# Kernel tuning notes

Hardware: AMD Instinct MI355X
Metric: run time of the kernel (lower is better)

## Reference

```python
import jax, jax.numpy as jnp
import numpy as np

B, S = 4, 2048
DM, H, DK, DV, DI = 512, 4, 128, 128, 1024
NT, NV = 64, 5000
PAD = 0


def layernorm(x, g, b, eps=1e-5):
    m = jnp.mean(x, axis=-1, keepdims=True)
    v = jnp.var(x, axis=-1, keepdims=True)
    return (x - m) * jax.lax.rsqrt(v + eps) * g + b


def setup_inputs() -> dict:
    key = jax.random.key(0)
    ks = jax.random.split(key, 20)
    event_type = jax.random.randint(ks[0], (B, S), 0, NT + 1)
    vertex = jax.random.randint(ks[1], (B, S), 0, NV + 1)
    vertex = jnp.where(event_type == PAD, 0, vertex)  # align padding
    event_time = jnp.sort(jax.random.uniform(ks[2], (B, S)) * 100.0, axis=1)
    non_pad_mask = (event_type != PAD).astype(jnp.float32)[..., None]  # [B,S,1]
    sc = 0.02
    event_emb = jax.random.normal(ks[3], (NT + 1, DM)) * sc
    event_emb = event_emb.at[PAD].set(0.0)
    vertex_emb = jax.random.normal(ks[4], (NV + 1, DM)) * sc
    vertex_emb = vertex_emb.at[PAD].set(0.0)
    A = jax.random.uniform(ks[5], (NV, NV))
    W = jax.random.uniform(ks[6], (NV, NV))
    Wq = jax.random.normal(ks[7], (DM, H * DK)) * sc
    Wk = jax.random.normal(ks[8], (DM, H * DK)) * sc
    Wv = jax.random.normal(ks[9], (DM, H * DV)) * sc
    Wo = jax.random.normal(ks[10], (H * DV, DM)) * sc
    bo = jnp.zeros((DM,))
    ln1_g, ln1_b = jnp.ones((DM,)), jnp.zeros((DM,))
    w1 = jax.random.normal(ks[11], (DM, DI)) * sc
    b1 = jnp.zeros((DI,))
    w2 = jax.random.normal(ks[12], (DI, DM)) * sc
    b2 = jnp.zeros((DM,))
    ln2_g, ln2_b = jnp.ones((DM,)), jnp.zeros((DM,))
    return dict(event_type=event_type, vertex=vertex, event_time=event_time,
                non_pad_mask=non_pad_mask, A=A, W=W, event_emb=event_emb,
                vertex_emb=vertex_emb, Wq=Wq, Wk=Wk, Wv=Wv, Wo=Wo, bo=bo,
                ln1_g=ln1_g, ln1_b=ln1_b, w1=w1, b1=b1, w2=w2, b2=b2,
                ln2_g=ln2_g, ln2_b=ln2_b)


def similarity(vertex, A, W):
    # vectorized form of the triple-loop pairwise gather: [B,1,S,S]
    idx = jnp.clip(vertex - 1, 0)                       # [B,S]
    vm = (vertex != 0)
    pair = vm[:, :, None] & vm[:, None, :]              # [B,S,S]
    sim = A[idx[:, :, None], idx[:, None, :]] * W[idx[:, :, None], idx[:, None, :]] * 10.0
    return (sim * pair.astype(A.dtype))[:, None]        # [B,1,S,S]


def temporal_enc(event_time, non_pad_mask, d_model):
    i = jnp.arange(d_model)
    pv = jnp.power(jnp.float32(10000.0), 2.0 * (i // 2).astype(jnp.float32) / d_model)
    r = event_time[:, :, None] / pv                     # [B,S,D]
    return jnp.where(i % 2 == 0, jnp.sin(r), jnp.cos(r)) * non_pad_mask


def reference(event_type, vertex, event_time, non_pad_mask, A, W, event_emb,
              vertex_emb, Wq, Wk, Wv, Wo, bo, ln1_g, ln1_b, w1, b1, w2, b2,
              ln2_g, ln2_b):
    b_, s_ = event_type.shape
    # masks: key-padding OR subsequent (causal)
    pad = (event_type == PAD)
    subseq = jnp.triu(jnp.ones((s_, s_), dtype=bool), 1)
    slf_attn_mask = pad[:, None, :] | subseq[None]      # [B,S,S]

    sim = similarity(vertex, A, W)                      # [B,1,S,S]
    tem = temporal_enc(event_time, non_pad_mask, DM)    # [B,S,D]
    ver = vertex_emb[vertex]                            # [B,S,D]
    enc = event_emb[event_type]                         # [B,S,D]

    # single encoder layer (n_layers=1), post-norm THP-style
    enc = enc + ver + tem
    res = enc
    q = (enc @ Wq).reshape(b_, s_, H, DK)
    k = (enc @ Wk).reshape(b_, s_, H, DK)
    v = (enc @ Wv).reshape(b_, s_, H, DV)
    scores = jnp.einsum('bihd,bjhd->bhij', q, k) / jnp.sqrt(jnp.float32(DK)) + sim
    scores = jnp.where(slf_attn_mask[:, None], jnp.float32(-1e9), scores)
    attn = jax.nn.softmax(scores, axis=-1)
    o = jnp.einsum('bhij,bjhd->bihd', attn, v).reshape(b_, s_, H * DV)
    o = o @ Wo + bo
    enc = layernorm(o + res, ln1_g, ln1_b) * non_pad_mask
    res = enc
    f = jax.nn.relu(enc @ w1 + b1) @ w2 + b2
    enc = layernorm(f + res, ln2_g, ln2_b) * non_pad_mask
    return enc, sim
```

## Files before the change

kernel.cpp:

```cpp
#include <hip/hip_runtime.h>
#include <hip/hip_bf16.h>

#define B_ 4
#define S_ 2048
#define DM_ 512
#define H_ 4
#define DK_ 128
#define DI_ 1024
#define NV_ 5000

typedef __attribute__((ext_vector_type(8))) short bf16x8;
typedef __attribute__((ext_vector_type(8))) unsigned short u16x8;
typedef __attribute__((ext_vector_type(4))) unsigned short u16x4;
typedef __attribute__((ext_vector_type(4))) float f32x4;

__device__ inline unsigned short f2bf(float x) {
  unsigned int u = __float_as_uint(x);
  unsigned int r = (u + 0x7fffu + ((u >> 16) & 1u)) >> 16;
  return (unsigned short)r;
}
__device__ inline float bf2f(unsigned short u) {
  return __uint_as_float(((unsigned int)u) << 16);
}
__device__ inline void gload16(const void* g, void* l) {
  __builtin_amdgcn_global_load_lds(
      (const __attribute__((address_space(1))) void*)g,
      (__attribute__((address_space(3))) void*)l, 16, 0, 0);
}

__global__ __launch_bounds__(256) void ew_kernel(
    const int* __restrict__ et, const int* __restrict__ vx,
    const float* __restrict__ tmv, const float* __restrict__ npm,
    const float* __restrict__ eemb, const float* __restrict__ vemb,
    const float* __restrict__ Wq, const float* __restrict__ Wk,
    const float* __restrict__ Wv, const float* __restrict__ Wo,
    const float* __restrict__ w1, const float* __restrict__ w2,
    float* __restrict__ enc0, unsigned short* __restrict__ enc0b,
    unsigned short* __restrict__ WqT, unsigned short* __restrict__ WkT,
    unsigned short* __restrict__ WvT, unsigned short* __restrict__ WoT,
    unsigned short* __restrict__ w1T, unsigned short* __restrict__ w2T) {
  __shared__ unsigned short T[32][40];
  int bid = blockIdx.x;
  int tid = threadIdx.x;
  if (bid < 8192) {
    int row = bid;
    int t = et[row], v = vx[row];
    float time = tmv[row], mask = npm[row];
    #pragma unroll
    for (int k = 0; k < 2; ++k) {
      int dd = tid + k * 256;
      float pvinv = __expf((float)(dd & ~1) * -0.017988946039015984f);
      float r = time * pvinv;
      float tem = (((dd & 1) == 0) ? sinf(r) : cosf(r)) * mask;
      float val = eemb[(size_t)t * DM_ + dd] + vemb[(size_t)v * DM_ + dd] + tem;
      enc0[(size_t)row * DM_ + dd] = val;
      enc0b[(size_t)row * DM_ + dd] = f2bf(val);
    }
  } else {
    int wb = bid - 8192;
    const float* src; unsigned short* dst; int K, N, lid;
    if (wb < 256)       { src = Wq; dst = WqT; K = 512;  N = 512;  lid = wb; }
    else if (wb < 512)  { src = Wk; dst = WkT; K = 512;  N = 512;  lid = wb - 256; }
    else if (wb < 768)  { src = Wv; dst = WvT; K = 512;  N = 512;  lid = wb - 512; }
    else if (wb < 1024) { src = Wo; dst = WoT; K = 512;  N = 512;  lid = wb - 768; }
    else if (wb < 1536) { src = w1; dst = w1T; K = 512;  N = 1024; lid = wb - 1024; }
    else                { src = w2; dst = w2T; K = 1024; N = 512;  lid = wb - 1536; }
    int nt = N / 32;
    int n0 = (lid % nt) * 32, k0 = (lid / nt) * 32;
    int r = tid >> 3, c0 = (tid & 7) * 4;
    float4 v = *(const float4*)&src[(size_t)(k0 + r) * N + n0 + c0];
    T[r][c0 + 0] = f2bf(v.x);
    T[r][c0 + 1] = f2bf(v.y);
    T[r][c0 + 2] = f2bf(v.z);
    T[r][c0 + 3] = f2bf(v.w);
    __syncthreads();
    u16x4 o;
    o[0] = T[c0 + 0][r]; o[1] = T[c0 + 1][r];
    o[2] = T[c0 + 2][r]; o[3] = T[c0 + 3][r];
    *(u16x4*)&dst[(size_t)(n0 + r) * K + k0 + c0] = o;
  }
}

__global__ __launch_bounds__(256) void simqkv_kernel(
    const int* __restrict__ vx, const float* __restrict__ A,
    const float* __restrict__ W, float* __restrict__ sim,
    const unsigned short* __restrict__ enc0b, const unsigned short* __restrict__ BT,
    unsigned short* __restrict__ QKV) {
  __shared__ __attribute__((aligned(16))) char arena[40960];
  int bid = blockIdx.x;
  int tid = threadIdx.x;
  int g = bid / 19, rr = bid % 19;
  if (rr < 16) {
    int job = g * 16 + rr;
    float* Ar = (float*)arena;
    float* Wr = (float*)(arena + 20480);
    int i = job & 2047;
    int b = job >> 11;
    int vi = vx[b * S_ + i];
    float* out = sim + ((size_t)(b * S_ + i)) * S_;
    if (vi == 0) {
      for (int j = tid * 4; j < S_; j += 1024)
        *(float4*)&out[j] = (float4){0.f, 0.f, 0.f, 0.f};
      return;
    }
    int w = tid >> 6, l = tid & 63;
    const char* Abase = (const char*)(A + (size_t)(vi - 1) * NV_);
    const char* Wbase = (const char*)(W + (size_t)(vi - 1) * NV_);
    #pragma unroll
    for (int it = 0; it < 5; ++it) {
      int seg = it * 4 + w;
      int chunk = seg * 64 + l;
      if (chunk < 1250) {
        gload16(Abase + (size_t)chunk * 16, (char*)Ar + seg * 1024);
        gload16(Wbase + (size_t)chunk * 16, (char*)Wr + seg * 1024);
      }
    }
    asm volatile("s_waitcnt vmcnt(0)" ::: "memory");
    __syncthreads();
    for (int j = tid * 4; j < S_; j += 1024) {
      int4 vj = *(const int4*)&vx[b * S_ + j];
      float4 o;
      o.x = vj.x ? Ar[vj.x - 1] * Wr[vj.x - 1] * 10.0f : 0.f;
      o.y = vj.y ? Ar[vj.y - 1] * Wr[vj.y - 1] * 10.0f : 0.f;
      o.z = vj.z ? Ar[vj.z - 1] * Wr[vj.z - 1] * 10.0f : 0.f;
      o.w = vj.w ? Ar[vj.w - 1] * Wr[vj.w - 1] * 10.0f : 0.f;
      *(float4*)&out[j] = o;
    }
  } else {
    unsigned short* As = (unsigned short*)arena;
    unsigned short* Bs = (unsigned short*)(arena + 9216);
    int qb = g * 3 + (rr - 16);
    int bx = qb % 12, by = qb / 12;
    int w = tid >> 6, l = tid & 63;
    int l16 = l & 15, lh = l >> 4;
    int row0 = by * 64, col0 = bx * 128;
    int ra = tid >> 1, ha = (tid & 1) * 32;
    int ra2 = tid >> 2, ha2 = (tid & 3) * 16;
    f32x4 acc[4][2];
    #pragma unroll
    for (int m = 0; m < 4; ++m)
      #pragma unroll
      for (int n = 0; n < 2; ++n) acc[m][n] = (f32x4){0.f, 0.f, 0.f, 0.f};

    for (int k0 = 0; k0 < 512; k0 += 64) {
      __syncthreads();
      {
        const unsigned short* sa = &enc0b[(size_t)(row0 + ra2) * 512 + k0 + ha2];
        uint4 a0 = *(const uint4*)(sa);
        uint4 a1 = *(const uint4*)(sa + 8);
        *(uint4*)&As[ra2 * 72 + ha2 + 0] = a0;
        *(uint4*)&As[ra2 * 72 + ha2 + 8] = a1;
        const unsigned short* sb = &BT[(size_t)(col0 + ra) * 512 + k0 + ha];
        uint4 b0 = *(const uint4*)(sb);
        uint4 b1 = *(const uint4*)(sb + 8);
        uint4 b2 = *(const uint4*)(sb + 16);
        uint4 b3 = *(const uint4*)(sb + 24);
        *(uint4*)&Bs[ra * 72 + ha + 0] = b0;
        *(uint4*)&Bs[ra * 72 + ha + 8] = b1;
        *(uint4*)&Bs[ra * 72 + ha + 16] = b2;
        *(uint4*)&Bs[ra * 72 + ha + 24] = b3;
      }
      __syncthreads();
      #pragma unroll
      for (int kc = 0; kc < 2; ++kc) {
        bf16x8 af[4], bfr[2];
        #pragma unroll
        for (int m = 0; m < 4; ++m)
          af[m] = *(bf16x8*)&As[(m * 16 + l16) * 72 + kc * 32 + lh * 8];
        #pragma unroll
        for (int n = 0; n < 2; ++n)
          bfr[n] = *(bf16x8*)&Bs[(w * 32 + n * 16 + l16) * 72 + kc * 32 + lh * 8];
        #pragma unroll
        for (int m = 0; m < 4; ++m)
          #pragma unroll
          for (int n = 0; n < 2; ++n)
            acc[m][n] = __builtin_amdgcn_mfma_f32_16x16x32_bf16(af[m], bfr[n], acc[m][n], 0, 0, 0);
      }
    }
    #pragma unroll
    for (int m = 0; m < 4; ++m) {
      #pragma unroll
      for (int r = 0; r < 4; ++r) {
        int row = row0 + m * 16 + lh * 4 + r;
        #pragma unroll
        for (int n = 0; n < 2; ++n) {
          int colg = col0 + w * 32 + n * 16 + l16;
          float v = acc[m][n][r];
          int which = colg >> 9;
          int cl = colg & 511;
          int b = row >> 11, s = row & 2047;
          int h = cl >> 7, d = cl & 127;
          unsigned short* base = QKV + (size_t)which * 4194304;
          if (which < 2)
            base[((size_t)((b * 4 + h) * 2048 + s)) * 128 + d] = f2bf(v);
          else
            base[((size_t)((b * 4 + h) * 128 + d)) * 2048 + s] = f2bf(v);
        }
      }
    }
  }
}

template <int OMODE, bool RELU, int MT = 128>
__global__ __launch_bounds__(256) void gemm_bf16_kernel(
    const unsigned short* __restrict__ A, const unsigned short* __restrict__ BT,
    const float* __restrict__ bias, void* __restrict__ C,
    int M, int N, int K) {
  __shared__ __attribute__((aligned(16))) unsigned short As[MT][72];
  __shared__ __attribute__((aligned(16))) unsigned short Bs[128][72];
  int tid = threadIdx.x;
  int w = tid >> 6, l = tid & 63;
  int l16 = l & 15, lh = l >> 4;
  const int NFR = (MT == 128) ? 4 : 2;
  int wr = (MT == 128) ? (w >> 1) : 0;
  int wc = (MT == 128) ? (w & 1) : w;
  int row0 = blockIdx.y * MT, col0 = blockIdx.x * 128;
  int ra = tid >> 1, ha = (tid & 1) * 32;
  f32x4 acc[4][4];
  #pragma unroll
  for (int m = 0; m < 4; ++m)
    #pragma unroll
    for (int n = 0; n < NFR; ++n) acc[m][n] = (f32x4){0.f, 0.f, 0.f, 0.f};

  for (int k0 = 0; k0 < K; k0 += 64) {
    __syncthreads();
    if (MT == 128) {
      const unsigned short* sa = &A[(size_t)(row0 + ra) * K + k0 + ha];
      uint4 a0 = *(const uint4*)(sa);
      uint4 a1 = *(const uint4*)(sa + 8);
      uint4 a2 = *(const uint4*)(sa + 16);
      uint4 a3 = *(const uint4*)(sa + 24);
      *(uint4*)&As[ra][ha + 0] = a0;
      *(uint4*)&As[ra][ha + 8] = a1;
      *(uint4*)&As[ra][ha + 16] = a2;
      *(uint4*)&As[ra][ha + 24] = a3;
    } else {
      int ra2 = tid >> 2, ha2 = (tid & 3) * 16;
      const unsigned short* sa = &A[(size_t)(row0 + ra2) * K + k0 + ha2];
      uint4 a0 = *(const uint4*)(sa);
      uint4 a1 = *(const uint4*)(sa + 8);
      *(uint4*)&As[ra2][ha2 + 0] = a0;
      *(uint4*)&As[ra2][ha2 + 8] = a1;
    }
    {
      const unsigned short* sb = &BT[(size_t)(col0 + ra) * K + k0 + ha];
      uint4 b0 = *(const uint4*)(sb);
      uint4 b1 = *(const uint4*)(sb + 8);
      uint4 b2 = *(const uint4*)(sb + 16);
      uint4 b3 = *(const uint4*)(sb + 24);
      *(uint4*)&Bs[ra][ha + 0] = b0;
      *(uint4*)&Bs[ra][ha + 8] = b1;
      *(uint4*)&Bs[ra][ha + 16] = b2;
      *(uint4*)&Bs[ra][ha + 24] = b3;
    }
    __syncthreads();
    #pragma unroll
    for (int kc = 0; kc < 2; ++kc) {
      bf16x8 af[4], bfr[4];
      #pragma unroll
      for (int m = 0; m < 4; ++m)
        af[m] = *(bf16x8*)&As[wr * 64 + m * 16 + l16][kc * 32 + lh * 8];
      #pragma unroll
      for (int n = 0; n < NFR; ++n)
        bfr[n] = *(bf16x8*)&Bs[wc * (16 * NFR) + n * 16 + l16][kc * 32 + lh * 8];
      #pragma unroll
      for (int m = 0; m < 4; ++m)
        #pragma unroll
        for (int n = 0; n < NFR; ++n)
          acc[m][n] = __builtin_amdgcn_mfma_f32_16x16x32_bf16(af[m], bfr[n], acc[m][n], 0, 0, 0);
    }
  }
  #pragma unroll
  for (int m = 0; m < 4; ++m) {
    #pragma unroll
    for (int r = 0; r < 4; ++r) {
      int row = row0 + wr * 64 + m * 16 + lh * 4 + r;
      #pragma unroll
      for (int n = 0; n < NFR; ++n) {
        int colg = col0 + wc * (16 * NFR) + n * 16 + l16;
        float v = acc[m][n][r];
        if (bias) v += bias[colg];
        if (RELU) v = fmaxf(v, 0.f);
        if (OMODE == 0) {
          ((float*)C)[(size_t)row * N + colg] = v;
        } else {
          ((unsigned short*)C)[(size_t)row * N + colg] = f2bf(v);
        }
      }
    }
  }
}

__global__ __launch_bounds__(256) void attn_mfma_kernel(
    const unsigned short* __restrict__ Qb, const unsigned short* __restrict__ Kb,
    const unsigned short* __restrict__ Vt, const float* __restrict__ sim,
    const float* __restrict__ npm, unsigned short* __restrict__ Op0,
    unsigned short* __restrict__ Op1, float2* __restrict__ ml0,
    float2* __restrict__ ml1) {
  __shared__ __attribute__((aligned(16))) char KsL[2][16384];
  __shared__ __attribute__((aligned(16))) char VtsL[2][16384];
  __shared__ __attribute__((aligned(16))) unsigned short Pl[4][16][72];
  int bid = blockIdx.x;
  int xcd = bid & 7;
  int j0 = bid >> 3;
  int bh = xcd * 2 + (j0 & 1);
  int jj = j0 >> 1;
  int pair = jj & 15;
  int half = jj >> 4;
  int b = bh >> 2;
  int tid = threadIdx.x;
  int w = tid >> 6, l = tid & 63;
  int l16 = l & 15, lh = l >> 4;
  unsigned short* Op = half ? Op1 : Op0;
  float2* ml = half ? ml1 : ml0;

  const char* KbB = (const char*)Kb + (size_t)bh * 2048 * 256;
  const char* VtB = (const char*)Vt + (size_t)bh * 128 * 4096;
  int krow[4], kcol[4], vrow4[4], vcol[4];
  #pragma unroll
  for (int j = 0; j < 4; ++j) {
    int i = w * 4 + j;
    krow[j] = i * 4 + (l >> 4);
    kcol[j] = ((l & 15) * 16) ^ ((krow[j] & 7) << 4);
    vrow4[j] = i * 8 + (l >> 3);
    vcol[j] = ((l & 7) * 16) ^ ((vrow4[j] & 7) << 4);
  }
  int xr = (l16 & 7) << 4;

  #pragma unroll 1
  for (int pj = 0; pj < 2; ++pj) {
    int qt = pj ? 31 - pair : pair;
    int nst = qt + 1;
    int c0 = (nst + 1) >> 1;
    int t0 = half ? c0 : 0;
    int cnt = half ? nst - c0 : c0;
    int q0 = qt * 64 + w * 16;
    int qg = q0 + l16;

    bf16x8 qf[4];
    const unsigned short* Qrow = Qb + ((size_t)(bh * 2048 + qg)) * 128;
    #pragma unroll
    for (int kq = 0; kq < 4; ++kq)
      qf[kq] = *(const bf16x8*)&Qrow[kq * 32 + lh * 8];

    float m_l = -INFINITY, l_l = 0.f;
    f32x4 o_acc[8];
    #pragma unroll
    for (int c = 0; c < 8; ++c) o_acc[c] = (f32x4){0.f, 0.f, 0.f, 0.f};

    const float* simrow = sim + ((size_t)(b * 2048) + qg) * 2048;
    const float* mrow = npm + b * 2048;

    if (cnt > 0) {
      #pragma unroll
      for (int j = 0; j < 4; ++j) {
        int i = w * 4 + j;
        gload16(KbB + (size_t)(t0 * 64 + krow[j]) * 256 + kcol[j],
                &KsL[0][i * 1024]);
        gload16(VtB + (size_t)vrow4[j] * 4096 + (size_t)(t0 * 64) * 2 + vcol[j],
                &VtsL[0][i * 1024]);
      }
      asm volatile("s_waitcnt vmcnt(0)" ::: "memory");
      __syncthreads();

      #pragma unroll 1
      for (int ti = 0; ti < cnt; ++ti) {
        int cur = ti & 1;
        int kv0 = (t0 + ti) * 64;
        if (ti + 1 < cnt) {
          int kvn = kv0 + 64;
          #pragma unroll
          for (int j = 0; j < 4; ++j) {
            int i = w * 4 + j;
            gload16(KbB + (size_t)(kvn + krow[j]) * 256 + kcol[j],
                    &KsL[cur ^ 1][i * 1024]);
            gload16(VtB + (size_t)vrow4[j] * 4096 + (size_t)kvn * 2 + vcol[j],
                    &VtsL[cur ^ 1][i * 1024]);
          }
        }
        const char* Kbase = KsL[cur];
        f32x4 sc[4];
        #pragma unroll
        for (int tt = 0; tt < 4; ++tt) {
          sc[tt] = (f32x4){0.f, 0.f, 0.f, 0.f};
          const char* Krow = Kbase + (tt * 16 + l16) * 256;
          #pragma unroll
          for (int kq = 0; kq < 4; ++kq) {
            bf16x8 kf = *(const bf16x8*)(Krow + ((kq * 64 + lh * 16) ^ xr));
            sc[tt] = __builtin_amdgcn_mfma_f32_16x16x32_bf16(kf, qf[kq], sc[tt], 0, 0, 0);
          }
        }
        float4 sim4[4], mk4[4];
        #pragma unroll
        for (int tt = 0; tt < 4; ++tt) {
          sim4[tt] = *(const float4*)&simrow[kv0 + tt * 16 + lh * 4];
          mk4[tt] = *(const float4*)&mrow[kv0 + tt * 16 + lh * 4];
        }
        float sv[4][4];
        #pragma unroll
        for (int tt = 0; tt < 4; ++tt) {
          #pragma unroll
          for (int r = 0; r < 4; ++r) {
            int kvg = kv0 + tt * 16 + lh * 4 + r;
            float mkr = r == 0 ? mk4[tt].x : r == 1 ? mk4[tt].y
                      : r == 2 ? mk4[tt].z : mk4[tt].w;
            float smr = r == 0 ? sim4[tt].x : r == 1 ? sim4[tt].y
                      : r == 2 ? sim4[tt].z : sim4[tt].w;
            bool valid = (kvg <= qg) && (mkr != 0.f);
            sv[tt][r] = valid ? sc[tt][r] * 0.08838834764831845f + smr : -1e9f;
          }
        }
        float mx = sv[0][0];
        #pragma unroll
        for (int tt = 0; tt < 4; ++tt)
          #pragma unroll
          for (int r = 0; r < 4; ++r) mx = fmaxf(mx, sv[tt][r]);
        mx = fmaxf(mx, __shfl_xor(mx, 16));
        mx = fmaxf(mx, __shfl_xor(mx, 32));
        float mn = fmaxf(m_l, mx);
        float alpha = __expf(m_l - mn);
        m_l = mn;
        float ts = 0.f;
        #pragma unroll
        for (int tt = 0; tt < 4; ++tt)
          #pragma unroll
          for (int r = 0; r < 4; ++r) {
            float ppv = __expf(sv[tt][r] - mn);
            sv[tt][r] = ppv;
            ts += ppv;
          }
        ts += __shfl_xor(ts, 16);
        ts += __shfl_xor(ts, 32);
        l_l = l_l * alpha + ts;
        #pragma unroll
        for (int tt = 0; tt < 4; ++tt) {
          u16x4 pw;
          pw[0] = f2bf(sv[tt][0]); pw[1] = f2bf(sv[tt][1]);
          pw[2] = f2bf(sv[tt][2]); pw[3] = f2bf(sv[tt][3]);
          *(u16x4*)&Pl[w][l16][tt * 16 + lh * 4] = pw;
        }
        float al[4];
        #pragma unroll
        for (int r = 0; r < 4; ++r) al[r] = __shfl(alpha, lh * 4 + r);
        #pragma unroll
        for (int c = 0; c < 8; ++c)
          #pragma unroll
          for (int r = 0; r < 4; ++r) o_acc[c][r] *= al[r];
        const char* Vbase = VtsL[cur];
        #pragma unroll
        for (int kf2 = 0; kf2 < 2; ++kf2) {
          bf16x8 pa = *(bf16x8*)&Pl[w][l16][kf2 * 32 + lh * 8];
          #pragma unroll
          for (int c = 0; c < 8; ++c) {
            bf16x8 vf = *(const bf16x8*)(Vbase + (c * 16 + l16) * 128 +
                                         ((kf2 * 64 + lh * 16) ^ xr));
            o_acc[c] = __builtin_amdgcn_mfma_f32_16x16x32_bf16(pa, vf, o_acc[c], 0, 0, 0);
          }
        }
        asm volatile("s_waitcnt vmcnt(0)" ::: "memory");
        __syncthreads();
      }
    }
    #pragma unroll
    for (int r = 0; r < 4; ++r) {
      int qgr = q0 + lh * 4 + r;
      unsigned short* op = Op + ((size_t)(bh * 2048 + qgr)) * 128;
      #pragma unroll
      for (int c = 0; c < 8; ++c) op[c * 16 + l16] = f2bf(o_acc[c][r]);
    }
    if (lh == 0) {
      float2 v; v.x = m_l; v.y = l_l;
      ml[bh * 2048 + q0 + l16] = v;
    }
    __syncthreads();
  }
}

__global__ __launch_bounds__(256) void attn_combine_kernel(
    const unsigned short* __restrict__ Op0, const unsigned short* __restrict__ Op1,
    const float2* __restrict__ ml0, const float2* __restrict__ ml1,
    unsigned short* __restrict__ Of) {
  int idx = blockIdx.x * 256 + threadIdx.x;
  int row = idx >> 4;
  int d0 = (idx & 15) * 8;
  float2 a = ml0[row], c2 = ml1[row];
  float m = fmaxf(a.x, c2.x);
  float e1 = __expf(a.x - m), e2 = __expf(c2.x - m);
  float inv = 1.f / (e1 * a.y + e2 * c2.y);
  u16x8 o1 = *(const u16x8*)&Op0[(size_t)row * 128 + d0];
  u16x8 o2 = *(const u16x8*)&Op1[(size_t)row * 128 + d0];
  int bh = row >> 11, q = row & 2047;
  int b = bh >> 2, h = bh & 3;
  unsigned short* dst = Of + ((size_t)(b * 2048 + q)) * 512 + h * 128 + d0;
  u16x8 o;
  #pragma unroll
  for (int j = 0; j < 8; ++j)
    o[j] = f2bf((bf2f(o1[j]) * e1 + bf2f(o2[j]) * e2) * inv);
  *(u16x8*)dst = o;
}

__global__ __launch_bounds__(256) void ln_kernel(
    const float* __restrict__ x, const float* __restrict__ res,
    const float* __restrict__ g, const float* __restrict__ bta,
    const float* __restrict__ npm, float* __restrict__ out,
    unsigned short* __restrict__ out16) {
  __shared__ float ssum[4], ssq[4];
  int row = blockIdx.x;
  int tid = threadIdx.x;
  size_t base = (size_t)row * DM_;
  float v0 = x[base + tid] + res[base + tid];
  float v1 = x[base + tid + 256] + res[base + tid + 256];
  float sum = v0 + v1, sq = v0 * v0 + v1 * v1;
  #pragma unroll
  for (int off = 32; off >= 1; off >>= 1) {
    sum += __shfl_down(sum, off);
    sq += __shfl_down(sq, off);
  }
  int wid = tid >> 6, lane = tid & 63;
  if (lane == 0) { ssum[wid] = sum; ssq[wid] = sq; }
  __syncthreads();
  sum = ssum[0] + ssum[1] + ssum[2] + ssum[3];
  sq = ssq[0] + ssq[1] + ssq[2] + ssq[3];
  float mean = sum * (1.f / DM_);
  float var = sq * (1.f / DM_) - mean * mean;
  float rs = rsqrtf(var + 1e-5f);
  float mask = npm[row];
  float o0 = ((v0 - mean) * rs * g[tid] + bta[tid]) * mask;
  float o1 = ((v1 - mean) * rs * g[tid + 256] + bta[tid + 256]) * mask;
  out[base + tid] = o0;
  out[base + tid + 256] = o1;
  if (out16) {
    out16[base + tid] = f2bf(o0);
    out16[base + tid + 256] = f2bf(o1);
  }
}

extern "C" void kernel_launch(void* const* d_in, const int* in_sizes, int n_in,
                              void* d_out, int out_size, void* d_ws,
                              size_t ws_size, hipStream_t stream) {
  const int* et = (const int*)d_in[0];
  const int* vx = (const int*)d_in[1];
  const float* tmv = (const float*)d_in[2];
  const float* npm = (const float*)d_in[3];
  const float* Amat = (const float*)d_in[4];
  const float* Wmat = (const float*)d_in[5];
  const float* eemb = (const float*)d_in[6];
  const float* vemb = (const float*)d_in[7];
  const float* Wq = (const float*)d_in[8];
  const float* Wk = (const float*)d_in[9];
  const float* Wv = (const float*)d_in[10];
  const float* Wo = (const float*)d_in[11];
  const float* bo = (const float*)d_in[12];
  const float* ln1g = (const float*)d_in[13];
  const float* ln1b = (const float*)d_in[14];
  const float* w1 = (const float*)d_in[15];
  const float* b1 = (const float*)d_in[16];
  const float* w2 = (const float*)d_in[17];
  const float* b2 = (const float*)d_in[18];
  const float* ln2g = (const float*)d_in[19];
  const float* ln2b = (const float*)d_in[20];

  float* out = (float*)d_out;
  float* enc_out = out;
  float* sim_out = out + (size_t)B_ * S_ * DM_;

  const size_t MB = 1ull << 20;
  char* wsb = (char*)d_ws;
  float* enc0 = (float*)(wsb + 0);
  unsigned short* enc0b = (unsigned short*)(wsb + 16 * MB);
  unsigned short* WqT = (unsigned short*)(wsb + 24 * MB);
  unsigned short* WkT = WqT + 512 * 512;
  unsigned short* WvT = WkT + 512 * 512;
  unsigned short* WoT = WvT + 512 * 512;
  unsigned short* w1T = WoT + 512 * 512;
  unsigned short* w2T = w1T + 1024 * 512;
  unsigned short* Qb16 = (unsigned short*)(wsb + 28 * MB);
  unsigned short* Kb16 = (unsigned short*)(wsb + 36 * MB);
  unsigned short* Vt16 = (unsigned short*)(wsb + 44 * MB);
  unsigned short* Op0 = (unsigned short*)(wsb + 52 * MB);
  unsigned short* Op1 = enc0b;
  float2* ml0 = (float2*)(wsb + 60 * MB);
  float2* ml1 = ml0 + 32768;
  unsigned short* Of16 = Qb16;
  float* OP = (float*)(wsb + 88 * MB);
  float* enc1 = OP;
  unsigned short* enc1b = enc0b;
  unsigned short* hid = Kb16;
  float* fbuf = (float*)(wsb + 52 * MB);

  int M = B_ * S_;

  ew_kernel<<<dim3(10240), dim3(256), 0, stream>>>(
      et, vx, tmv, npm, eemb, vemb, Wq, Wk, Wv, Wo, w1, w2,
      enc0, enc0b, WqT, WkT, WvT, WoT, w1T, w2T);

  simqkv_kernel<<<dim3(9728), dim3(256), 0, stream>>>(
      vx, Amat, Wmat, sim_out, enc0b, WqT, Qb16);

  attn_mfma_kernel<<<dim3(512), dim3(256), 0, stream>>>(
      Qb16, Kb16, Vt16, sim_out, npm, Op0, Op1, ml0, ml1);
  attn_combine_kernel<<<dim3(2048), dim3(256), 0, stream>>>(
      Op0, Op1, ml0, ml1, Of16);

  gemm_bf16_kernel<0, false, 64><<<dim3(4, 128), dim3(256), 0, stream>>>(
      Of16, WoT, bo, OP, M, DM_, DM_);
  ln_kernel<<<dim3(M), dim3(256), 0, stream>>>(OP, enc0, ln1g, ln1b, npm, enc1,
                                               enc1b);

  gemm_bf16_kernel<1, true, 64><<<dim3(8, 128), dim3(256), 0, stream>>>(
      enc1b, w1T, b1, hid, M, DI_, DM_);
  gemm_bf16_kernel<0, false, 64><<<dim3(4, 128), dim3(256), 0, stream>>>(
      hid, w2T, b2, fbuf, M, DM_, DI_);
  ln_kernel<<<dim3(M), dim3(256), 0, stream>>>(fbuf, enc1, ln2g, ln2b, npm,
                                               enc_out, nullptr);
}
```

Before: 260.1 us.

## Precompute bf16 A*W*10 table and gather sim rows from it

Adds extra blocks to the elementwise kernel that multiply the whole 5000x5000 A and W matrices (times 10) and store the result as a bf16 table in the workspace. The similarity path then stages one bf16 row per query into LDS instead of two fp32 rows, cutting per-row gather traffic by a factor of four. In exchange it streams both full matrices every call even though only rows for present vertices are needed. It also rounds the returned sim output to bf16 precision. When the workspace is too small, it falls back to a direct global gather with no LDS staging.

```diff
diff --git a/kernel.cpp b/kernel.cpp
--- a/kernel.cpp
+++ b/kernel.cpp
@@ -35,10 +35,12 @@
     const float* __restrict__ Wq, const float* __restrict__ Wk,
     const float* __restrict__ Wv, const float* __restrict__ Wo,
     const float* __restrict__ w1, const float* __restrict__ w2,
+    const float* __restrict__ A, const float* __restrict__ W,
     float* __restrict__ enc0, unsigned short* __restrict__ enc0b,
     unsigned short* __restrict__ WqT, unsigned short* __restrict__ WkT,
     unsigned short* __restrict__ WvT, unsigned short* __restrict__ WoT,
-    unsigned short* __restrict__ w1T, unsigned short* __restrict__ w2T) {
+    unsigned short* __restrict__ w1T, unsigned short* __restrict__ w2T,
+    unsigned short* __restrict__ AWb, int useAW) {
   __shared__ unsigned short T[32][40];
   int bid = blockIdx.x;
   int tid = threadIdx.x;
@@ -56,7 +58,7 @@
       enc0[(size_t)row * DM_ + dd] = val;
       enc0b[(size_t)row * DM_ + dd] = f2bf(val);
     }
-  } else {
+  } else if (bid < 10240) {
     int wb = bid - 8192;
     const float* src; unsigned short* dst; int K, N, lid;
     if (wb < 256)       { src = Wq; dst = WqT; K = 512;  N = 512;  lid = wb; }
@@ -78,22 +80,36 @@
     o[0] = T[c0 + 0][r]; o[1] = T[c0 + 1][r];
     o[2] = T[c0 + 2][r]; o[3] = T[c0 + 3][r];
     *(u16x4*)&dst[(size_t)(n0 + r) * K + k0 + c0] = o;
+  } else {
+    if (!useAW) return;
+    size_t base = ((size_t)(bid - 10240) * 256 + tid) * 8;
+    if (base < (size_t)NV_ * NV_) {
+      float4 a0 = *(const float4*)&A[base];
+      float4 a1 = *(const float4*)&A[base + 4];
+      float4 w0 = *(const float4*)&W[base];
+      float4 w1v = *(const float4*)&W[base + 4];
+      u16x8 o;
+      o[0] = f2bf(a0.x * w0.x * 10.f); o[1] = f2bf(a0.y * w0.y * 10.f);
+      o[2] = f2bf(a0.z * w0.z * 10.f); o[3] = f2bf(a0.w * w0.w * 10.f);
+      o[4] = f2bf(a1.x * w1v.x * 10.f); o[5] = f2bf(a1.y * w1v.y * 10.f);
+      o[6] = f2bf(a1.z * w1v.z * 10.f); o[7] = f2bf(a1.w * w1v.w * 10.f);
+      *(u16x8*)&AWb[base] = o;
+    }
   }
 }
 
 __global__ __launch_bounds__(256) void simqkv_kernel(
     const int* __restrict__ vx, const float* __restrict__ A,
-    const float* __restrict__ W, float* __restrict__ sim,
-    const unsigned short* __restrict__ enc0b, const unsigned short* __restrict__ BT,
-    unsigned short* __restrict__ QKV) {
-  __shared__ __attribute__((aligned(16))) char arena[40960];
+    const float* __restrict__ W, const unsigned short* __restrict__ AWb,
+    float* __restrict__ sim, const unsigned short* __restrict__ enc0b,
+    const unsigned short* __restrict__ BT, unsigned short* __restrict__ QKV,
+    int useAW) {
+  __shared__ __attribute__((aligned(16))) char arena[28672];
   int bid = blockIdx.x;
   int tid = threadIdx.x;
   int g = bid / 19, rr = bid % 19;
   if (rr < 16) {
     int job = g * 16 + rr;
-    float* Ar = (float*)arena;
-    float* Wr = (float*)(arena + 20480);
     int i = job & 2047;
     int b = job >> 11;
     int vi = vx[b * S_ + i];
@@ -103,28 +119,40 @@
         *(float4*)&out[j] = (float4){0.f, 0.f, 0.f, 0.f};
       return;
     }
-    int w = tid >> 6, l = tid & 63;
-    const char* Abase = (const char*)(A + (size_t)(vi - 1) * NV_);
-    const char* Wbase = (const char*)(W + (size_t)(vi - 1) * NV_);
-    #pragma unroll
-    for (int it = 0; it < 5; ++it) {
-      int seg = it * 4 + w;
-      int chunk = seg * 64 + l;
-      if (chunk < 1250) {
-        gload16(Abase + (size_t)chunk * 16, (char*)Ar + seg * 1024);
-        gload16(Wbase + (size_t)chunk * 16, (char*)Wr + seg * 1024);
-      }
-    }
-    asm volatile("s_waitcnt vmcnt(0)" ::: "memory");
-    __syncthreads();
-    for (int j = tid * 4; j < S_; j += 1024) {
-      int4 vj = *(const int4*)&vx[b * S_ + j];
-      float4 o;
-      o.x = vj.x ? Ar[vj.x - 1] * Wr[vj.x - 1] * 10.0f : 0.f;
-      o.y = vj.y ? Ar[vj.y - 1] * Wr[vj.y - 1] * 10.0f : 0.f;
-      o.z = vj.z ? Ar[vj.z - 1] * Wr[vj.z - 1] * 10.0f : 0.f;
-      o.w = vj.w ? Ar[vj.w - 1] * Wr[vj.w - 1] * 10.0f : 0.f;
-      *(float4*)&out[j] = o;
+    if (useAW) {
+      unsigned short* AWr = (unsigned short*)arena;
+      int w = tid >> 6, l = tid & 63;
+      const char* AWbase = (const char*)(AWb + (size_t)(vi - 1) * NV_);
+      #pragma unroll
+      for (int it = 0; it < 3; ++it) {
+        int seg = it * 4 + w;
+        int chunk = seg * 64 + l;
+        if (chunk < 625)
+          gload16(AWbase + (size_t)chunk * 16, (char*)AWr + seg * 1024);
+      }
+      asm volatile("s_waitcnt vmcnt(0)" ::: "memory");
+      __syncthreads();
+      for (int j = tid * 4; j < S_; j += 1024) {
+        int4 vj = *(const int4*)&vx[b * S_ + j];
+        float4 o;
+        o.x = vj.x ? bf2f(AWr[vj.x - 1]) : 0.f;
+        o.y = vj.y ? bf2f(AWr[vj.y - 1]) : 0.f;
+        o.z = vj.z ? bf2f(AWr[vj.z - 1]) : 0.f;
+        o.w = vj.w ? bf2f(AWr[vj.w - 1]) : 0.f;
+        *(float4*)&out[j] = o;
+      }
+    } else {
+      const float* Arow = A + (size_t)(vi - 1) * NV_;
+      const float* Wrow = W + (size_t)(vi - 1) * NV_;
+      for (int j = tid * 4; j < S_; j += 1024) {
+        int4 vj = *(const int4*)&vx[b * S_ + j];
+        float4 o;
+        o.x = vj.x ? Arow[vj.x - 1] * Wrow[vj.x - 1] * 10.0f : 0.f;
+        o.y = vj.y ? Arow[vj.y - 1] * Wrow[vj.y - 1] * 10.0f : 0.f;
+        o.z = vj.z ? Arow[vj.z - 1] * Wrow[vj.z - 1] * 10.0f : 0.f;
+        o.w = vj.w ? Arow[vj.w - 1] * Wrow[vj.w - 1] * 10.0f : 0.f;
+        *(float4*)&out[j] = o;
+      }
     }
   } else {
     unsigned short* As = (unsigned short*)arena;
@@ -587,15 +615,18 @@
   unsigned short* enc1b = enc0b;
   unsigned short* hid = Kb16;
   float* fbuf = (float*)(wsb + 52 * MB);
+  unsigned short* AWb = (unsigned short*)(wsb + 104 * MB);
+  int useAW = (ws_size >= 104 * MB + (size_t)NV_ * NV_ * 2) ? 1 : 0;
 
   int M = B_ * S_;
 
-  ew_kernel<<<dim3(10240), dim3(256), 0, stream>>>(
-      et, vx, tmv, npm, eemb, vemb, Wq, Wk, Wv, Wo, w1, w2,
-      enc0, enc0b, WqT, WkT, WvT, WoT, w1T, w2T);
+  int ewBlocks = 10240 + (useAW ? 12208 : 0);
+  ew_kernel<<<dim3(ewBlocks), dim3(256), 0, stream>>>(
+      et, vx, tmv, npm, eemb, vemb, Wq, Wk, Wv, Wo, w1, w2, Amat, Wmat,
+      enc0, enc0b, WqT, WkT, WvT, WoT, w1T, w2T, AWb, useAW);
 
   simqkv_kernel<<<dim3(9728), dim3(256), 0, stream>>>(
-      vx, Amat, Wmat, sim_out, enc0b, WqT, Qb16);
+      vx, Amat, Wmat, AWb, sim_out, enc0b, WqT, Qb16, useAW);
 
   attn_mfma_kernel<<<dim3(512), dim3(256), 0, stream>>>(
       Qb16, Kb16, Vt16, sim_out, npm, Op0, Op1, ml0, ml1);
```

Result: slower. 285.3 us (+9.7%).
